# Kernel optimization log

Hardware: AMD Instinct MI355X
Metric: run time of the kernel (lower is better)

Reference implementation:

```python
import jax, jax.numpy as jnp
import numpy as np

B, S, IN, H, OUT, L = 64, 512, 512, 1024, 512, 2


def setup_inputs() -> dict:
    key = jax.random.key(0)
    ks = jax.random.split(key, 12)
    s_in = 1.0 / np.sqrt(IN)
    s_h = 1.0 / np.sqrt(H)
    inp = {
        "x": jax.random.normal(ks[0], (B, S, IN), dtype=jnp.float32),
        "h0": jnp.zeros((B, L, H), dtype=jnp.float32),
        # layer 0: gates stacked [z; r; g] along first axis
        "Wx0": jax.random.uniform(ks[1], (3 * H, IN), minval=-s_in, maxval=s_in),
        "Wh0": jax.random.uniform(ks[2], (3 * H, H), minval=-s_h, maxval=s_h),
        "bh0": jax.random.uniform(ks[3], (3 * H,), minval=-s_h, maxval=s_h),
        # layer 1 (input dim is H)
        "Wx1": jax.random.uniform(ks[4], (3 * H, H), minval=-s_h, maxval=s_h),
        "Wh1": jax.random.uniform(ks[5], (3 * H, H), minval=-s_h, maxval=s_h),
        "bh1": jax.random.uniform(ks[6], (3 * H,), minval=-s_h, maxval=s_h),
        # output projection fc_hy
        "Why": jax.random.uniform(ks[7], (OUT, H), minval=-s_h, maxval=s_h),
        "by": jax.random.uniform(ks[8], (OUT,), minval=-s_h, maxval=s_h),
    }
    return inp


def _gru_layer(x, h_init, Wx, Wh, bh):
    """x: [B,S,D], h_init: [B,H]. Returns (ys [B,S,H], h_final [B,H])."""
    # Batch the input-side projections for all timesteps at once.
    xp = jnp.einsum("bsd,gd->bsg", x, Wx)  # [B,S,3H]
    xz, xr, xg = jnp.split(xp, 3, axis=-1)
    Whz, Whr, Whg = jnp.split(Wh, 3, axis=0)
    bhz, bhr, bhg = jnp.split(bh, 3, axis=0)

    def step(h, xs):
        xz_t, xr_t, xg_t = xs  # each [B,H]
        z = jax.nn.sigmoid(xz_t + h @ Whz.T + bhz)
        r = jax.nn.sigmoid(xr_t + h @ Whr.T + bhr)
        g = jnp.tanh(xg_t + (r * h) @ Whg.T + bhg)
        h_new = z * h + (1.0 - z) * g
        return h_new, h_new

    # time-major scan
    xs = (xz.transpose(1, 0, 2), xr.transpose(1, 0, 2), xg.transpose(1, 0, 2))
    h_final, ys = jax.lax.scan(step, h_init, xs)
    return ys.transpose(1, 0, 2), h_final  # [B,S,H], [B,H]


def reference(x, h0, Wx0, Wh0, bh0, Wx1, Wh1, bh1, Why, by):
    # dropout rate is 0 -> dropout is identity
    y0, hf0 = _gru_layer(x, h0[:, 0, :], Wx0, Wh0, bh0)
    y1, hf1 = _gru_layer(y0, h0[:, 1, :], Wx1, Wh1, bh1)
    layer_output = jnp.einsum("bsh,oh->bso", y1, Why) + by  # [B,S,OUT]
    hidden_state = jnp.stack([hf0, hf1], axis=1)  # [B,L,H]
    return layer_output, jax.lax.stop_gradient(hidden_state)
```

## Files before the change

### kernel.cpp

```cpp
#include <hip/hip_runtime.h>
#include <hip/hip_bf16.h>

#define B_   64
#define S_   512
#define IN_  512
#define H_   1024
#define OUT_ 512
#define H3_  3072
#define TC_  32
#define TCL2 5
#define NCHUNK (S_ / TC_)
#define MC_  (B_ * TC_)
#define NROW (B_ * S_)

#define NBLK 128
#define NTHR 512
#define EXN  32768
#define FPAD 16
#define STAGE_OFF 0
#define HOWN_OFF  32768
#define ZOWN_OFF  36928
#define SMEM_BYTES 41088

typedef float f32x4 __attribute__((ext_vector_type(4)));
typedef short bf16x8 __attribute__((ext_vector_type(8)));
typedef unsigned int u32;
typedef u32 u32x4 __attribute__((ext_vector_type(4)));

struct ChainArgs {
  const float* xp;
  const __hip_bfloat16* Wh;
  float* hf;
  u32* hbuf;
  u32* rhbuf;
  u32* fA;
  u32* fB;
  __hip_bfloat16* y;
  u32 baseA, baseB;
  int t0;
  int layer;
  int active;
  int stagger;
};

__device__ __forceinline__ u32 f2bf_bits(float v) {
  union { __hip_bfloat16 b; unsigned short s; } cv;
  cv.b = __float2bfloat16(v);
  return (u32)cv.s;
}

__device__ __forceinline__ void coh_st(u32* p, u32 v) {
  __hip_atomic_store(p, v, __ATOMIC_RELAXED, __HIP_MEMORY_SCOPE_AGENT);
}
__device__ __forceinline__ u32 coh_ld(const u32* p) {
  return __hip_atomic_load(p, __ATOMIC_RELAXED, __HIP_MEMORY_SCOPE_AGENT);
}

__device__ __forceinline__ void waitflags(const u32* f, int rgbase, u32 target) {
  const u32* my = f + (size_t)(rgbase + (threadIdx.x & 15)) * FPAD;
  int it = 0;
  while (true) {
    u32 v = coh_ld(my);
    if (__all((int)(v >= target))) break;
    if (it < 2) {
      __builtin_amdgcn_s_sleep(2);
    } else {
      __builtin_amdgcn_s_sleep(8);
    }
    ++it;
  }
  __builtin_amdgcn_sched_barrier(0);
}

__device__ __forceinline__ void stage_ex(const u32* __restrict__ src, char* stage, int tid,
                                         int rg) {
  u32x4 v[4];
#pragma unroll
  for (int i = 0; i < 4; ++i) {
    int c4 = tid + i * NTHR;
    int cgp = c4 >> 7;
    int s = c4 & 127;
    const u32* p = src + (((size_t)(cgp * 4 + rg) * 16 + (s >> 3)) * 32 + (s & 7) * 4);
    asm volatile("global_load_dwordx4 %0, %1, off sc0 sc1" : "=v"(v[i]) : "v"(p));
  }
  asm volatile("s_waitcnt vmcnt(0)" ::: "memory");
#pragma unroll
  for (int i = 0; i < 4; ++i) {
    int c4 = tid + i * NTHR;
    int cgp = c4 >> 7;
    int s = c4 & 127;
    int r = s >> 3;
    *(u32x4*)(stage + r * 2048 + ((cgp * 128 + (s & 7) * 16) ^ ((r & 7) << 4))) = v[i];
  }
}

__global__ __launch_bounds__(256) void cast_f32_to_bf16(const float* __restrict__ in,
                                                        __hip_bfloat16* __restrict__ out,
                                                        int n4) {
  int i = blockIdx.x * 256 + threadIdx.x;
  if (i >= n4) return;
  float4 v = ((const float4*)in)[i];
  out[4 * i + 0] = __float2bfloat16(v.x);
  out[4 * i + 1] = __float2bfloat16(v.y);
  out[4 * i + 2] = __float2bfloat16(v.z);
  out[4 * i + 3] = __float2bfloat16(v.w);
}

__global__ __launch_bounds__(256) void gather_cast_x(const float* __restrict__ x,
                                                     __hip_bfloat16* __restrict__ out, int t0) {
  int i = blockIdx.x * 256 + threadIdx.x;
  int e = i * 4;
  int b = e >> 14;
  int rem = e & 16383;
  float4 v = *(const float4*)(x + (size_t)b * (S_ * IN_) + (size_t)t0 * IN_ + rem);
  out[e + 0] = __float2bfloat16(v.x);
  out[e + 1] = __float2bfloat16(v.y);
  out[e + 2] = __float2bfloat16(v.z);
  out[e + 3] = __float2bfloat16(v.w);
}

template <bool REMAP>
__global__ __launch_bounds__(256) void gemm_nt_bias(const __hip_bfloat16* __restrict__ A,
                                                    const __hip_bfloat16* __restrict__ Bm,
                                                    const float* __restrict__ bias,
                                                    float* __restrict__ C, int M, int N, int K,
                                                    int t0) {
  const int lane = threadIdx.x & 63;
  const int w = threadIdx.x >> 6;
  const int wr = w >> 1, wc = w & 1;
  const int row0 = blockIdx.y * 128 + wr * 64;
  const int col0 = blockIdx.x * 128 + wc * 64;
  const int kl = (lane >> 4) * 8;
  const int m16 = lane & 15;
  f32x4 acc[4][4] = {};
  for (int k0 = 0; k0 < K; k0 += 32) {
    bf16x8 a[4], b[4];
#pragma unroll
    for (int i = 0; i < 4; ++i)
      a[i] = *(const bf16x8*)(A + (size_t)(row0 + i * 16 + m16) * K + k0 + kl);
#pragma unroll
    for (int j = 0; j < 4; ++j)
      b[j] = *(const bf16x8*)(Bm + (size_t)(col0 + j * 16 + m16) * K + k0 + kl);
#pragma unroll
    for (int i = 0; i < 4; ++i)
#pragma unroll
      for (int j = 0; j < 4; ++j)
        acc[i][j] = __builtin_amdgcn_mfma_f32_16x16x32_bf16(a[i], b[j], acc[i][j], 0, 0, 0);
  }
  const int rsub = (lane >> 4) * 4;
#pragma unroll
  for (int i = 0; i < 4; ++i) {
    int row = row0 + i * 16 + rsub;
#pragma unroll
    for (int j = 0; j < 4; ++j) {
      int col = col0 + j * 16 + m16;
      float bv = bias[col];
#pragma unroll
      for (int r = 0; r < 4; ++r) {
        int rr = row + r;
        int crow = REMAP ? ((rr >> TCL2) * S_ + t0 + (rr & (TC_ - 1))) : rr;
        C[(size_t)crow * N + col] = acc[i][j][r] + bv;
      }
    }
  }
}

__device__ __forceinline__ void chain_scan(const ChainArgs& ca, const float* __restrict__ h0,
                                           float* __restrict__ hid_out, char* smem, int bx) {
  char* stage = smem + STAGE_OFF;
  float* h_own = (float*)(smem + HOWN_OFF);
  float* z_own = (float*)(smem + ZOWN_OFF);

  const int tid = threadIdx.x;
  const int lane = tid & 63;
  const int w = tid >> 6;
  const int wc = w & 3;
  const int isR = w >> 2;
  const int rg = bx >> 4;
  const int cg = bx & 15;
  const int fid = bx;
  const int rgbase = rg * 16;
  const int m16 = lane & 15;
  const int kl = (lane >> 4) * 8;
  const int rsub = (lane >> 4) * 4;
  const int swzA = (m16 & 7) << 4;
  const int cloc = wc * 16 + m16;

  const float* xp = ca.xp;
  const __hip_bfloat16* Wh = ca.Wh;
  u32* hbuf = ca.hbuf;
  u32* rhbuf = ca.rhbuf;
  u32* flagA = ca.fA;
  u32* flagB = ca.fB;
  const u32 baseA = ca.baseA, baseB = ca.baseB;
  const int t0 = ca.t0, layer = ca.layer;

  for (int i = 0; i < ca.stagger; ++i) __builtin_amdgcn_s_sleep(16);

  {
    int row = tid >> 5, pp = tid & 31;
    int col = cg * 64 + pp * 2;
    int grow = rg * 16 + row;
    float v0, v1;
    if (t0 == 0) {
      v0 = h0[((size_t)grow * 2 + layer) * H_ + col];
      v1 = h0[((size_t)grow * 2 + layer) * H_ + col + 1];
      coh_st(hbuf + EXN + (((size_t)(cg * 4 + rg) * 16 + row) * 32 + pp),
             f2bf_bits(v0) | (f2bf_bits(v1) << 16));
    } else {
      v0 = ca.hf[grow * H_ + col];
      v1 = ca.hf[grow * H_ + col + 1];
    }
    h_own[row * 65 + pp * 2] = v0;
    h_own[row * 65 + pp * 2 + 1] = v1;
  }
  asm volatile("s_waitcnt vmcnt(0)" ::: "memory");
  __syncthreads();
  if (tid == 0) coh_st(flagB + (size_t)fid * FPAD, baseB + 1);

  for (int t = 0; t < TC_; ++t) {
    const int par = t & 1;
    const int colA = cg * 64 + cloc + (isR ? H_ : 0);
    float xpv[4], xpg[4];
#pragma unroll
    for (int j = 0; j < 4; ++j) {
      int grow = rg * 16 + rsub + j;
      xpv[j] = xp[((size_t)(grow * TC_ + t)) * H3_ + colA];
    }
    if (w < 4) {
#pragma unroll
      for (int j = 0; j < 4; ++j) {
        int grow = rg * 16 + rsub + j;
        xpg[j] = xp[((size_t)(grow * TC_ + t)) * H3_ + 2 * H_ + cg * 64 + cloc];
      }
    }

    waitflags(flagB, rgbase, baseB + 1 + t);
    stage_ex(hbuf + (par ^ 1) * EXN, stage, tid, rg);
    __syncthreads();
    {
      f32x4 acc0 = {}, acc1 = {};
      const char* abase = stage + m16 * 2048;
      const __hip_bfloat16* Bb = Wh + (size_t)colA * H_;
#pragma unroll
      for (int k0 = 0; k0 < H_; k0 += 64) {
        bf16x8 a0 = *(const bf16x8*)(abase + (((k0 + kl) * 2) ^ swzA));
        bf16x8 a1 = *(const bf16x8*)(abase + (((k0 + 32 + kl) * 2) ^ swzA));
        bf16x8 b0 = *(const bf16x8*)(Bb + k0 + kl);
        bf16x8 b1 = *(const bf16x8*)(Bb + k0 + 32 + kl);
        acc0 = __builtin_amdgcn_mfma_f32_16x16x32_bf16(a0, b0, acc0, 0, 0, 0);
        acc1 = __builtin_amdgcn_mfma_f32_16x16x32_bf16(a1, b1, acc1, 0, 0, 0);
      }
      if (!isR) {
#pragma unroll
        for (int j = 0; j < 4; ++j) {
          float pre = acc0[j] + acc1[j] + xpv[j];
          z_own[(rsub + j) * 65 + cloc] = 1.f / (1.f + expf(-pre));
        }
      } else {
#pragma unroll
        for (int j = 0; j < 4; ++j) {
          int lr = rsub + j;
          float pre = acc0[j] + acc1[j] + xpv[j];
          float s = 1.f / (1.f + expf(-pre));
          float rh = s * h_own[lr * 65 + cloc];
          u32 bits = f2bf_bits(rh);
          u32 pair = bits | (((u32)__shfl_down((int)bits, 1)) << 16);
          if ((m16 & 1) == 0)
            coh_st(rhbuf + par * EXN + (((size_t)(cg * 4 + rg) * 16 + lr) * 32 + (cloc >> 1)),
                   pair);
        }
        asm volatile("s_waitcnt vmcnt(0)" ::: "memory");
      }
    }
    __syncthreads();
    if (tid == 0) coh_st(flagA + (size_t)fid * FPAD, baseA + t + 1);

    waitflags(flagA, rgbase, baseA + t + 1);
    stage_ex(rhbuf + par * EXN, stage, tid, rg);
    __syncthreads();
    if (w < 4) {
      f32x4 acc0 = {}, acc1 = {};
      const char* abase = stage + m16 * 2048;
      const __hip_bfloat16* Bb = Wh + (size_t)(2 * H_ + cg * 64 + cloc) * H_;
#pragma unroll
      for (int k0 = 0; k0 < H_; k0 += 64) {
        bf16x8 a0 = *(const bf16x8*)(abase + (((k0 + kl) * 2) ^ swzA));
        bf16x8 a1 = *(const bf16x8*)(abase + (((k0 + 32 + kl) * 2) ^ swzA));
        bf16x8 b0 = *(const bf16x8*)(Bb + k0 + kl);
        bf16x8 b1 = *(const bf16x8*)(Bb + k0 + 32 + kl);
        acc0 = __builtin_amdgcn_mfma_f32_16x16x32_bf16(a0, b0, acc0, 0, 0, 0);
        acc1 = __builtin_amdgcn_mfma_f32_16x16x32_bf16(a1, b1, acc1, 0, 0, 0);
      }
#pragma unroll
      for (int j = 0; j < 4; ++j) {
        int lr = rsub + j;
        float pre = acc0[j] + acc1[j] + xpg[j];
        float gg = tanhf(pre);
        float zz = z_own[lr * 65 + cloc];
        float hv = h_own[lr * 65 + cloc];
        float hn = zz * hv + (1.f - zz) * gg;
        h_own[lr * 65 + cloc] = hn;
        u32 bits = f2bf_bits(hn);
        u32 pair = bits | (((u32)__shfl_down((int)bits, 1)) << 16);
        if ((m16 & 1) == 0)
          coh_st(hbuf + par * EXN + (((size_t)(cg * 4 + rg) * 16 + lr) * 32 + (cloc >> 1)), pair);
        ca.y[((size_t)((rg * 16 + lr) * TC_ + t)) * H_ + cg * 64 + cloc] = __float2bfloat16(hn);
      }
      asm volatile("s_waitcnt vmcnt(0)" ::: "memory");
    }
    __syncthreads();
    if (tid == 0) coh_st(flagB + (size_t)fid * FPAD, baseB + t + 2);
  }

  {
    int row = tid >> 5, pp = tid & 31;
    int col = cg * 64 + pp * 2;
    int grow = rg * 16 + row;
    float v0 = h_own[row * 65 + pp * 2];
    float v1 = h_own[row * 65 + pp * 2 + 1];
    ca.hf[grow * H_ + col] = v0;
    ca.hf[grow * H_ + col + 1] = v1;
    if (t0 + TC_ == S_) {
      hid_out[((size_t)grow * 2 + layer) * H_ + col] = v0;
      hid_out[((size_t)grow * 2 + layer) * H_ + col + 1] = v1;
    }
  }
}

__global__ __launch_bounds__(NTHR) void gru_scan_fused(ChainArgs a0, ChainArgs a1,
                                                       const float* __restrict__ h0,
                                                       float* __restrict__ hid_out) {
  extern __shared__ char smem[];
  if (blockIdx.x < 64) {
    if (!a0.active) return;
    chain_scan(a0, h0, hid_out, smem, blockIdx.x);
  } else {
    if (!a1.active) return;
    chain_scan(a1, h0, hid_out, smem, blockIdx.x - 64);
  }
}

extern "C" void kernel_launch(void* const* d_in, const int* in_sizes, int n_in,
                              void* d_out, int out_size, void* d_ws, size_t ws_size,
                              hipStream_t stream) {
  const float* x   = (const float*)d_in[0];
  const float* h0  = (const float*)d_in[1];
  const float* Wx0 = (const float*)d_in[2];
  const float* Wh0 = (const float*)d_in[3];
  const float* bh0 = (const float*)d_in[4];
  const float* Wx1 = (const float*)d_in[5];
  const float* Wh1 = (const float*)d_in[6];
  const float* bh1 = (const float*)d_in[7];
  const float* Why = (const float*)d_in[8];
  const float* by  = (const float*)d_in[9];
  float* out = (float*)d_out;
  float* hid_out = out + (size_t)NROW * OUT_;

  (void)hipFuncSetAttribute((const void*)gru_scan_fused,
                            hipFuncAttributeMaxDynamicSharedMemorySize, SMEM_BYTES);

  char* ws = (char*)d_ws;
  size_t off = 0;
  auto alloc = [&](size_t bytes) {
    char* p = ws + off;
    off += (bytes + 255) & ~(size_t)255;
    return p;
  };
  __hip_bfloat16* wx0b = (__hip_bfloat16*)alloc((size_t)H3_ * IN_ * 2);
  __hip_bfloat16* wh0b = (__hip_bfloat16*)alloc((size_t)H3_ * H_ * 2);
  __hip_bfloat16* wx1b = (__hip_bfloat16*)alloc((size_t)H3_ * H_ * 2);
  __hip_bfloat16* wh1b = (__hip_bfloat16*)alloc((size_t)H3_ * H_ * 2);
  __hip_bfloat16* whyb = (__hip_bfloat16*)alloc((size_t)OUT_ * H_ * 2);
  float* h_f32_0 = (float*)alloc((size_t)B_ * H_ * 4);
  float* h_f32_1 = (float*)alloc((size_t)B_ * H_ * 4);
  u32* hbuf_0  = (u32*)alloc((size_t)2 * EXN * 4);
  u32* hbuf_1  = (u32*)alloc((size_t)2 * EXN * 4);
  u32* rhbuf_0 = (u32*)alloc((size_t)2 * EXN * 4);
  u32* rhbuf_1 = (u32*)alloc((size_t)2 * EXN * 4);
  __hip_bfloat16* x_bfc = (__hip_bfloat16*)alloc((size_t)MC_ * IN_ * 2);
  __hip_bfloat16* y0buf = (__hip_bfloat16*)alloc((size_t)MC_ * H_ * 2);
  __hip_bfloat16* y1buf = (__hip_bfloat16*)alloc((size_t)MC_ * H_ * 2);
  float* xp0buf = (float*)alloc((size_t)MC_ * H3_ * 4);
  float* xp1buf = (float*)alloc((size_t)MC_ * H3_ * 4);
  u32* flags    = (u32*)alloc(4 * 256 * FPAD * 4);
  (void)ws_size;

  (void)hipMemsetAsync(flags, 0, 4 * 256 * FPAD * 4, stream);

  auto cast = [&](const float* in, __hip_bfloat16* o, size_t n) {
    cast_f32_to_bf16<<<dim3((unsigned)((n / 4 + 255) / 256)), dim3(256), 0, stream>>>(in, o,
                                                                                     (int)(n / 4));
  };
  cast(Wx0, wx0b, (size_t)H3_ * IN_);
  cast(Wh0, wh0b, (size_t)H3_ * H_);
  cast(Wx1, wx1b, (size_t)H3_ * H_);
  cast(Wh1, wh1b, (size_t)H3_ * H_);
  cast(Why, whyb, (size_t)OUT_ * H_);

  u32* fA0 = flags;
  u32* fB0 = flags + 256 * FPAD;
  u32* fA1 = flags + 512 * FPAD;
  u32* fB1 = flags + 768 * FPAD;

  auto mkchain = [&](int layer, int chunk, int active) {
    ChainArgs ca;
    int cc = chunk < 0 ? 0 : chunk;
    ca.xp = layer == 0 ? xp0buf : xp1buf;
    ca.Wh = layer == 0 ? wh0b : wh1b;
    ca.hf = layer == 0 ? h_f32_0 : h_f32_1;
    ca.hbuf = layer == 0 ? hbuf_0 : hbuf_1;
    ca.rhbuf = layer == 0 ? rhbuf_0 : rhbuf_1;
    ca.fA = layer == 0 ? fA0 : fA1;
    ca.fB = layer == 0 ? fB0 : fB1;
    ca.y = layer == 0 ? y0buf : y1buf;
    ca.baseA = (u32)cc * TC_;
    ca.baseB = (u32)cc * (TC_ + 1);
    ca.t0 = cc * TC_;
    ca.layer = layer;
    ca.active = active;
    ca.stagger = (layer == 1) ? 14 : 0;
    return ca;
  };

  gather_cast_x<<<dim3(MC_ * IN_ / 4 / 256), dim3(256), 0, stream>>>(x, x_bfc, 0);
  gemm_nt_bias<false><<<dim3(H3_ / 128, MC_ / 128), dim3(256), 0, stream>>>(
      x_bfc, wx0b, bh0, xp0buf, MC_, H3_, IN_, 0);

  for (int c = 0; c <= NCHUNK; ++c) {
    ChainArgs a0 = mkchain(0, c, c < NCHUNK ? 1 : 0);
    ChainArgs a1 = mkchain(1, c - 1, c > 0 ? 1 : 0);
    {
      void* args[] = {(void*)&a0, (void*)&a1, (void*)&h0, (void*)&hid_out};
      hipError_t e = hipLaunchCooperativeKernel((void*)gru_scan_fused, dim3(NBLK), dim3(NTHR),
                                                args, SMEM_BYTES, stream);
      if (e != hipSuccess) {
        (void)hipGetLastError();
        gru_scan_fused<<<dim3(NBLK), dim3(NTHR), SMEM_BYTES, stream>>>(a0, a1, h0, hid_out);
      }
    }
    if (c < NCHUNK) {
      gemm_nt_bias<false><<<dim3(H3_ / 128, MC_ / 128), dim3(256), 0, stream>>>(
          y0buf, wx1b, bh1, xp1buf, MC_, H3_, H_, 0);
    }
    if (c + 1 < NCHUNK) {
      gather_cast_x<<<dim3(MC_ * IN_ / 4 / 256), dim3(256), 0, stream>>>(x, x_bfc, (c + 1) * TC_);
      gemm_nt_bias<false><<<dim3(H3_ / 128, MC_ / 128), dim3(256), 0, stream>>>(
          x_bfc, wx0b, bh0, xp0buf, MC_, H3_, IN_, 0);
    }
    if (c > 0) {
      gemm_nt_bias<true><<<dim3(OUT_ / 128, MC_ / 128), dim3(256), 0, stream>>>(
          y1buf, whyb, by, out, MC_, OUT_, H_, (c - 1) * TC_);
    }
  }
}
```

Baseline: 10.82 ms.

## Stage exchanged hidden slices per producer on flag arrival instead of waiting for all

```diff
diff --git a/kernel.cpp b/kernel.cpp
--- a/kernel.cpp
+++ b/kernel.cpp
@@ -36,6 +36,8 @@
   u32* fA;
   u32* fB;
   __hip_bfloat16* y;
+  const float* h0;
+  float* hid_out;
   u32 baseA, baseB;
   int t0;
   int layer;
@@ -52,46 +54,41 @@
 __device__ __forceinline__ void coh_st(u32* p, u32 v) {
   __hip_atomic_store(p, v, __ATOMIC_RELAXED, __HIP_MEMORY_SCOPE_AGENT);
 }
-__device__ __forceinline__ u32 coh_ld(const u32* p) {
-  return __hip_atomic_load(p, __ATOMIC_RELAXED, __HIP_MEMORY_SCOPE_AGENT);
-}
-
-__device__ __forceinline__ void waitflags(const u32* f, int rgbase, u32 target) {
-  const u32* my = f + (size_t)(rgbase + (threadIdx.x & 15)) * FPAD;
-  int it = 0;
-  while (true) {
-    u32 v = coh_ld(my);
-    if (__all((int)(v >= target))) break;
-    if (it < 2) {
-      __builtin_amdgcn_s_sleep(2);
-    } else {
-      __builtin_amdgcn_s_sleep(8);
-    }
-    ++it;
+
+__device__ __forceinline__ void stage_arrival(const u32* __restrict__ f, int rgbase, u32 target,
+                                              const u32* __restrict__ src, char* stage, int rg) {
+  const int lane = threadIdx.x & 63;
+  const int w = threadIdx.x >> 6;
+#pragma unroll
+  for (int pi = 0; pi < 2; ++pi) {
+    const int p = 2 * w + pi;
+    const u32* fp = f + (size_t)(rgbase + p) * FPAD;
+    int it = 0;
+    while (true) {
+      u32 v;
+      asm volatile("global_load_dword %0, %1, off sc0 sc1\n\ts_waitcnt vmcnt(0)"
+                   : "=v"(v) : "v"(fp) : "memory");
+      if (__all((int)(v >= target))) break;
+      if (it < 4) {
+        __builtin_amdgcn_s_sleep(1);
+      } else {
+        __builtin_amdgcn_s_sleep(4);
+      }
+      ++it;
+    }
+    const u32* sp = src + ((size_t)(p * 4 + rg) * 16) * 32;
+    u32x4 v0, v1;
+    asm volatile("global_load_dwordx4 %0, %1, off sc0 sc1" : "=v"(v0) : "v"(sp + (size_t)lane * 4));
+    asm volatile("global_load_dwordx4 %0, %1, off sc0 sc1"
+                 : "=v"(v1) : "v"(sp + (size_t)(lane + 64) * 4));
+    asm volatile("s_waitcnt vmcnt(0)" ::: "memory");
+    int k = lane, r = k >> 3;
+    *(u32x4*)(stage + r * 2048 + ((p * 128 + (k & 7) * 16) ^ ((r & 7) << 4))) = v0;
+    k = lane + 64;
+    r = k >> 3;
+    *(u32x4*)(stage + r * 2048 + ((p * 128 + (k & 7) * 16) ^ ((r & 7) << 4))) = v1;
   }
   __builtin_amdgcn_sched_barrier(0);
-}
-
-__device__ __forceinline__ void stage_ex(const u32* __restrict__ src, char* stage, int tid,
-                                         int rg) {
-  u32x4 v[4];
-#pragma unroll
-  for (int i = 0; i < 4; ++i) {
-    int c4 = tid + i * NTHR;
-    int cgp = c4 >> 7;
-    int s = c4 & 127;
-    const u32* p = src + (((size_t)(cgp * 4 + rg) * 16 + (s >> 3)) * 32 + (s & 7) * 4);
-    asm volatile("global_load_dwordx4 %0, %1, off sc0 sc1" : "=v"(v[i]) : "v"(p));
-  }
-  asm volatile("s_waitcnt vmcnt(0)" ::: "memory");
-#pragma unroll
-  for (int i = 0; i < 4; ++i) {
-    int c4 = tid + i * NTHR;
-    int cgp = c4 >> 7;
-    int s = c4 & 127;
-    int r = s >> 3;
-    *(u32x4*)(stage + r * 2048 + ((cgp * 128 + (s & 7) * 16) ^ ((r & 7) << 4))) = v[i];
-  }
 }
 
 __global__ __launch_bounds__(256) void cast_f32_to_bf16(const float* __restrict__ in,
@@ -165,8 +162,7 @@
   }
 }
 
-__device__ __forceinline__ void chain_scan(const ChainArgs& ca, const float* __restrict__ h0,
-                                           float* __restrict__ hid_out, char* smem, int bx) {
+__device__ void chain_scan(const ChainArgs& ca, char* smem, int bx) {
   char* stage = smem + STAGE_OFF;
   float* h_own = (float*)(smem + HOWN_OFF);
   float* z_own = (float*)(smem + ZOWN_OFF);
@@ -203,8 +199,8 @@
     int grow = rg * 16 + row;
     float v0, v1;
     if (t0 == 0) {
-      v0 = h0[((size_t)grow * 2 + layer) * H_ + col];
-      v1 = h0[((size_t)grow * 2 + layer) * H_ + col + 1];
+      v0 = ca.h0[((size_t)grow * 2 + layer) * H_ + col];
+      v1 = ca.h0[((size_t)grow * 2 + layer) * H_ + col + 1];
       coh_st(hbuf + EXN + (((size_t)(cg * 4 + rg) * 16 + row) * 32 + pp),
              f2bf_bits(v0) | (f2bf_bits(v1) << 16));
     } else {
@@ -214,9 +210,11 @@
     h_own[row * 65 + pp * 2] = v0;
     h_own[row * 65 + pp * 2 + 1] = v1;
   }
-  asm volatile("s_waitcnt vmcnt(0)" ::: "memory");
-  __syncthreads();
-  if (tid == 0) coh_st(flagB + (size_t)fid * FPAD, baseB + 1);
+  if (t0 == 0) {
+    asm volatile("s_waitcnt vmcnt(0)" ::: "memory");
+    __syncthreads();
+    if (tid == 0) coh_st(flagB + (size_t)fid * FPAD, baseB + 1);
+  }
 
   for (int t = 0; t < TC_; ++t) {
     const int par = t & 1;
@@ -235,8 +233,7 @@
       }
     }
 
-    waitflags(flagB, rgbase, baseB + 1 + t);
-    stage_ex(hbuf + (par ^ 1) * EXN, stage, tid, rg);
+    stage_arrival(flagB, rgbase, baseB + 1 + t, hbuf + (par ^ 1) * EXN, stage, rg);
     __syncthreads();
     {
       f32x4 acc0 = {}, acc1 = {};
@@ -276,8 +273,7 @@
     __syncthreads();
     if (tid == 0) coh_st(flagA + (size_t)fid * FPAD, baseA + t + 1);
 
-    waitflags(flagA, rgbase, baseA + t + 1);
-    stage_ex(rhbuf + par * EXN, stage, tid, rg);
+    stage_arrival(flagA, rgbase, baseA + t + 1, rhbuf + par * EXN, stage, rg);
     __syncthreads();
     if (w < 4) {
       f32x4 acc0 = {}, acc1 = {};
@@ -322,22 +318,20 @@
     ca.hf[grow * H_ + col] = v0;
     ca.hf[grow * H_ + col + 1] = v1;
     if (t0 + TC_ == S_) {
-      hid_out[((size_t)grow * 2 + layer) * H_ + col] = v0;
-      hid_out[((size_t)grow * 2 + layer) * H_ + col + 1] = v1;
-    }
-  }
-}
-
-__global__ __launch_bounds__(NTHR) void gru_scan_fused(ChainArgs a0, ChainArgs a1,
-                                                       const float* __restrict__ h0,
-                                                       float* __restrict__ hid_out) {
+      ca.hid_out[((size_t)grow * 2 + layer) * H_ + col] = v0;
+      ca.hid_out[((size_t)grow * 2 + layer) * H_ + col + 1] = v1;
+    }
+  }
+}
+
+__global__ __launch_bounds__(NTHR) void gru_scan_fused(ChainArgs a0, ChainArgs a1) {
   extern __shared__ char smem[];
   if (blockIdx.x < 64) {
     if (!a0.active) return;
-    chain_scan(a0, h0, hid_out, smem, blockIdx.x);
+    chain_scan(a0, smem, blockIdx.x);
   } else {
     if (!a1.active) return;
-    chain_scan(a1, h0, hid_out, smem, blockIdx.x - 64);
+    chain_scan(a1, smem, blockIdx.x - 64);
   }
 }
 
@@ -414,8 +408,10 @@
     ca.fA = layer == 0 ? fA0 : fA1;
     ca.fB = layer == 0 ? fB0 : fB1;
     ca.y = layer == 0 ? y0buf : y1buf;
+    ca.h0 = h0;
+    ca.hid_out = hid_out;
     ca.baseA = (u32)cc * TC_;
-    ca.baseB = (u32)cc * (TC_ + 1);
+    ca.baseB = (u32)cc * TC_;
     ca.t0 = cc * TC_;
     ca.layer = layer;
     ca.active = active;
@@ -431,12 +427,12 @@
     ChainArgs a0 = mkchain(0, c, c < NCHUNK ? 1 : 0);
     ChainArgs a1 = mkchain(1, c - 1, c > 0 ? 1 : 0);
     {
-      void* args[] = {(void*)&a0, (void*)&a1, (void*)&h0, (void*)&hid_out};
+      void* args[] = {(void*)&a0, (void*)&a1};
       hipError_t e = hipLaunchCooperativeKernel((void*)gru_scan_fused, dim3(NBLK), dim3(NTHR),
                                                 args, SMEM_BYTES, stream);
       if (e != hipSuccess) {
         (void)hipGetLastError();
-        gru_scan_fused<<<dim3(NBLK), dim3(NTHR), SMEM_BYTES, stream>>>(a0, a1, h0, hid_out);
+        gru_scan_fused<<<dim3(NBLK), dim3(NTHR), SMEM_BYTES, stream>>>(a0, a1);
       }
     }
     if (c < NCHUNK) {
```

After: 10.99 ms. No clear change (+1.6%).

## Co-locate both GRU layer chains in one 1024-thread block with soft barriers

Applied to the files above, without the earlier changes.

```diff
diff --git a/kernel.cpp b/kernel.cpp
--- a/kernel.cpp
+++ b/kernel.cpp
@@ -13,14 +13,16 @@
 #define MC_  (B_ * TC_)
 #define NROW (B_ * S_)
 
-#define NBLK 128
-#define NTHR 512
+#define NBLK 64
+#define NTHR 1024
+#define CTHR 512
 #define EXN  32768
 #define FPAD 16
 #define STAGE_OFF 0
 #define HOWN_OFF  32768
 #define ZOWN_OFF  36928
-#define SMEM_BYTES 41088
+#define HALF_     41088
+#define SMEM_BYTES (2 * HALF_)
 
 typedef float f32x4 __attribute__((ext_vector_type(4)));
 typedef short bf16x8 __attribute__((ext_vector_type(8)));
@@ -36,6 +38,8 @@
   u32* fA;
   u32* fB;
   __hip_bfloat16* y;
+  const float* h0;
+  float* hid_out;
   u32 baseA, baseB;
   int t0;
   int layer;
@@ -52,15 +56,24 @@
 __device__ __forceinline__ void coh_st(u32* p, u32 v) {
   __hip_atomic_store(p, v, __ATOMIC_RELAXED, __HIP_MEMORY_SCOPE_AGENT);
 }
-__device__ __forceinline__ u32 coh_ld(const u32* p) {
-  return __hip_atomic_load(p, __ATOMIC_RELAXED, __HIP_MEMORY_SCOPE_AGENT);
-}
-
-__device__ __forceinline__ void waitflags(const u32* f, int rgbase, u32 target) {
-  const u32* my = f + (size_t)(rgbase + (threadIdx.x & 15)) * FPAD;
+
+__device__ __forceinline__ void soft_bar(u32* cnt, u32& bt) {
+  bt += 8;
+  asm volatile("s_waitcnt vmcnt(0) lgkmcnt(0)" ::: "memory");
+  if ((threadIdx.x & 63) == 0) atomicAdd(cnt, 1u);
+  while (__hip_atomic_load(cnt, __ATOMIC_RELAXED, __HIP_MEMORY_SCOPE_WORKGROUP) < bt) {
+    __builtin_amdgcn_s_sleep(1);
+  }
+  __builtin_amdgcn_sched_barrier(0);
+}
+
+__device__ __forceinline__ void waitflags(const u32* f, int rgbase, u32 target, int tl) {
+  const u32* my = f + (size_t)(rgbase + (tl & 15)) * FPAD;
   int it = 0;
   while (true) {
-    u32 v = coh_ld(my);
+    u32 v;
+    asm volatile("global_load_dword %0, %1, off sc0 sc1\n\ts_waitcnt vmcnt(0)"
+                 : "=v"(v) : "v"(my) : "memory");
     if (__all((int)(v >= target))) break;
     if (it < 2) {
       __builtin_amdgcn_s_sleep(2);
@@ -72,12 +85,12 @@
   __builtin_amdgcn_sched_barrier(0);
 }
 
-__device__ __forceinline__ void stage_ex(const u32* __restrict__ src, char* stage, int tid,
+__device__ __forceinline__ void stage_ex(const u32* __restrict__ src, char* stage, int tl,
                                          int rg) {
   u32x4 v[4];
 #pragma unroll
   for (int i = 0; i < 4; ++i) {
-    int c4 = tid + i * NTHR;
+    int c4 = tl + i * CTHR;
     int cgp = c4 >> 7;
     int s = c4 & 127;
     const u32* p = src + (((size_t)(cgp * 4 + rg) * 16 + (s >> 3)) * 32 + (s & 7) * 4);
@@ -86,7 +99,7 @@
   asm volatile("s_waitcnt vmcnt(0)" ::: "memory");
 #pragma unroll
   for (int i = 0; i < 4; ++i) {
-    int c4 = tid + i * NTHR;
+    int c4 = tl + i * CTHR;
     int cgp = c4 >> 7;
     int s = c4 & 127;
     int r = s >> 3;
@@ -165,15 +178,13 @@
   }
 }
 
-__device__ __forceinline__ void chain_scan(const ChainArgs& ca, const float* __restrict__ h0,
-                                           float* __restrict__ hid_out, char* smem, int bx) {
+__device__ void chain_scan(const ChainArgs& ca, char* smem, int bx, int tl, u32* cnt) {
   char* stage = smem + STAGE_OFF;
   float* h_own = (float*)(smem + HOWN_OFF);
   float* z_own = (float*)(smem + ZOWN_OFF);
 
-  const int tid = threadIdx.x;
-  const int lane = tid & 63;
-  const int w = tid >> 6;
+  const int lane = tl & 63;
+  const int w = tl >> 6;
   const int wc = w & 3;
   const int isR = w >> 2;
   const int rg = bx >> 4;
@@ -194,17 +205,18 @@
   u32* flagB = ca.fB;
   const u32 baseA = ca.baseA, baseB = ca.baseB;
   const int t0 = ca.t0, layer = ca.layer;
+  u32 bt = 0;
 
   for (int i = 0; i < ca.stagger; ++i) __builtin_amdgcn_s_sleep(16);
 
   {
-    int row = tid >> 5, pp = tid & 31;
+    int row = tl >> 5, pp = tl & 31;
     int col = cg * 64 + pp * 2;
     int grow = rg * 16 + row;
     float v0, v1;
     if (t0 == 0) {
-      v0 = h0[((size_t)grow * 2 + layer) * H_ + col];
-      v1 = h0[((size_t)grow * 2 + layer) * H_ + col + 1];
+      v0 = ca.h0[((size_t)grow * 2 + layer) * H_ + col];
+      v1 = ca.h0[((size_t)grow * 2 + layer) * H_ + col + 1];
       coh_st(hbuf + EXN + (((size_t)(cg * 4 + rg) * 16 + row) * 32 + pp),
              f2bf_bits(v0) | (f2bf_bits(v1) << 16));
     } else {
@@ -214,9 +226,8 @@
     h_own[row * 65 + pp * 2] = v0;
     h_own[row * 65 + pp * 2 + 1] = v1;
   }
-  asm volatile("s_waitcnt vmcnt(0)" ::: "memory");
-  __syncthreads();
-  if (tid == 0) coh_st(flagB + (size_t)fid * FPAD, baseB + 1);
+  soft_bar(cnt, bt);
+  if (tl == 0) coh_st(flagB + (size_t)fid * FPAD, baseB + 1);
 
   for (int t = 0; t < TC_; ++t) {
     const int par = t & 1;
@@ -235,9 +246,9 @@
       }
     }
 
-    waitflags(flagB, rgbase, baseB + 1 + t);
-    stage_ex(hbuf + (par ^ 1) * EXN, stage, tid, rg);
-    __syncthreads();
+    waitflags(flagB, rgbase, baseB + 1 + t, tl);
+    stage_ex(hbuf + (par ^ 1) * EXN, stage, tl, rg);
+    soft_bar(cnt, bt);
     {
       f32x4 acc0 = {}, acc1 = {};
       const char* abase = stage + m16 * 2048;
@@ -270,15 +281,14 @@
             coh_st(rhbuf + par * EXN + (((size_t)(cg * 4 + rg) * 16 + lr) * 32 + (cloc >> 1)),
                    pair);
         }
-        asm volatile("s_waitcnt vmcnt(0)" ::: "memory");
-      }
-    }
-    __syncthreads();
-    if (tid == 0) coh_st(flagA + (size_t)fid * FPAD, baseA + t + 1);
-
-    waitflags(flagA, rgbase, baseA + t + 1);
-    stage_ex(rhbuf + par * EXN, stage, tid, rg);
-    __syncthreads();
+      }
+    }
+    soft_bar(cnt, bt);
+    if (tl == 0) coh_st(flagA + (size_t)fid * FPAD, baseA + t + 1);
+
+    waitflags(flagA, rgbase, baseA + t + 1, tl);
+    stage_ex(rhbuf + par * EXN, stage, tl, rg);
+    soft_bar(cnt, bt);
     if (w < 4) {
       f32x4 acc0 = {}, acc1 = {};
       const char* abase = stage + m16 * 2048;
@@ -307,14 +317,13 @@
           coh_st(hbuf + par * EXN + (((size_t)(cg * 4 + rg) * 16 + lr) * 32 + (cloc >> 1)), pair);
         ca.y[((size_t)((rg * 16 + lr) * TC_ + t)) * H_ + cg * 64 + cloc] = __float2bfloat16(hn);
       }
-      asm volatile("s_waitcnt vmcnt(0)" ::: "memory");
-    }
-    __syncthreads();
-    if (tid == 0) coh_st(flagB + (size_t)fid * FPAD, baseB + t + 2);
+    }
+    soft_bar(cnt, bt);
+    if (tl == 0) coh_st(flagB + (size_t)fid * FPAD, baseB + t + 2);
   }
 
   {
-    int row = tid >> 5, pp = tid & 31;
+    int row = tl >> 5, pp = tl & 31;
     int col = cg * 64 + pp * 2;
     int grow = rg * 16 + row;
     float v0 = h_own[row * 65 + pp * 2];
@@ -322,22 +331,26 @@
     ca.hf[grow * H_ + col] = v0;
     ca.hf[grow * H_ + col + 1] = v1;
     if (t0 + TC_ == S_) {
-      hid_out[((size_t)grow * 2 + layer) * H_ + col] = v0;
-      hid_out[((size_t)grow * 2 + layer) * H_ + col + 1] = v1;
-    }
-  }
-}
-
-__global__ __launch_bounds__(NTHR) void gru_scan_fused(ChainArgs a0, ChainArgs a1,
-                                                       const float* __restrict__ h0,
-                                                       float* __restrict__ hid_out) {
+      ca.hid_out[((size_t)grow * 2 + layer) * H_ + col] = v0;
+      ca.hid_out[((size_t)grow * 2 + layer) * H_ + col + 1] = v1;
+    }
+  }
+}
+
+__global__ __launch_bounds__(NTHR) void gru_scan_fused(ChainArgs a0, ChainArgs a1) {
   extern __shared__ char smem[];
-  if (blockIdx.x < 64) {
+  __shared__ u32 bar_cnt[2];
+  const int tid = threadIdx.x;
+  if (tid < 2) bar_cnt[tid] = 0;
+  __syncthreads();
+  const int chain = tid >> 9;
+  const int tl = tid & 511;
+  if (chain == 0) {
     if (!a0.active) return;
-    chain_scan(a0, h0, hid_out, smem, blockIdx.x);
+    chain_scan(a0, smem, blockIdx.x, tl, &bar_cnt[0]);
   } else {
     if (!a1.active) return;
-    chain_scan(a1, h0, hid_out, smem, blockIdx.x - 64);
+    chain_scan(a1, smem + HALF_, blockIdx.x, tl, &bar_cnt[1]);
   }
 }
 
@@ -414,6 +427,8 @@
     ca.fA = layer == 0 ? fA0 : fA1;
     ca.fB = layer == 0 ? fB0 : fB1;
     ca.y = layer == 0 ? y0buf : y1buf;
+    ca.h0 = h0;
+    ca.hid_out = hid_out;
     ca.baseA = (u32)cc * TC_;
     ca.baseB = (u32)cc * (TC_ + 1);
     ca.t0 = cc * TC_;
@@ -431,12 +446,12 @@
     ChainArgs a0 = mkchain(0, c, c < NCHUNK ? 1 : 0);
     ChainArgs a1 = mkchain(1, c - 1, c > 0 ? 1 : 0);
     {
-      void* args[] = {(void*)&a0, (void*)&a1, (void*)&h0, (void*)&hid_out};
+      void* args[] = {(void*)&a0, (void*)&a1};
       hipError_t e = hipLaunchCooperativeKernel((void*)gru_scan_fused, dim3(NBLK), dim3(NTHR),
                                                 args, SMEM_BYTES, stream);
       if (e != hipSuccess) {
         (void)hipGetLastError();
-        gru_scan_fused<<<dim3(NBLK), dim3(NTHR), SMEM_BYTES, stream>>>(a0, a1, h0, hid_out);
+        gru_scan_fused<<<dim3(NBLK), dim3(NTHR), SMEM_BYTES, stream>>>(a0, a1);
       }
     }
     if (c < NCHUNK) {
```

Result: slower. 19.39 ms (+79.2%).

## Halve scan blocks so each block interleaves two row groups

Applied to the files above, without the earlier changes.

```diff
diff --git a/kernel.cpp b/kernel.cpp
--- a/kernel.cpp
+++ b/kernel.cpp
@@ -13,14 +13,16 @@
 #define MC_  (B_ * TC_)
 #define NROW (B_ * S_)
 
-#define NBLK 128
+#define NBLK 64
 #define NTHR 512
 #define EXN  32768
 #define FPAD 16
 #define STAGE_OFF 0
-#define HOWN_OFF  32768
-#define ZOWN_OFF  36928
-#define SMEM_BYTES 41088
+#define HOWN0_OFF 32768
+#define ZOWN0_OFF 36928
+#define HOWN1_OFF 41088
+#define ZOWN1_OFF 45248
+#define SMEM_BYTES 49408
 
 typedef float f32x4 __attribute__((ext_vector_type(4)));
 typedef short bf16x8 __attribute__((ext_vector_type(8)));
@@ -36,11 +38,12 @@
   u32* fA;
   u32* fB;
   __hip_bfloat16* y;
+  const float* h0;
+  float* hid_out;
   u32 baseA, baseB;
   int t0;
   int layer;
   int active;
-  int stagger;
 };
 
 __device__ __forceinline__ u32 f2bf_bits(float v) {
@@ -52,15 +55,14 @@
 __device__ __forceinline__ void coh_st(u32* p, u32 v) {
   __hip_atomic_store(p, v, __ATOMIC_RELAXED, __HIP_MEMORY_SCOPE_AGENT);
 }
-__device__ __forceinline__ u32 coh_ld(const u32* p) {
-  return __hip_atomic_load(p, __ATOMIC_RELAXED, __HIP_MEMORY_SCOPE_AGENT);
-}
 
 __device__ __forceinline__ void waitflags(const u32* f, int rgbase, u32 target) {
   const u32* my = f + (size_t)(rgbase + (threadIdx.x & 15)) * FPAD;
   int it = 0;
   while (true) {
-    u32 v = coh_ld(my);
+    u32 v;
+    asm volatile("global_load_dword %0, %1, off sc0 sc1\n\ts_waitcnt vmcnt(0)"
+                 : "=v"(v) : "v"(my) : "memory");
     if (__all((int)(v >= target))) break;
     if (it < 2) {
       __builtin_amdgcn_s_sleep(2);
@@ -165,21 +167,17 @@
   }
 }
 
-__device__ __forceinline__ void chain_scan(const ChainArgs& ca, const float* __restrict__ h0,
-                                           float* __restrict__ hid_out, char* smem, int bx) {
+__device__ void chain_scan(const ChainArgs& ca, char* smem, int p, int cg) {
   char* stage = smem + STAGE_OFF;
-  float* h_own = (float*)(smem + HOWN_OFF);
-  float* z_own = (float*)(smem + ZOWN_OFF);
+  float* h_own[2] = {(float*)(smem + HOWN0_OFF), (float*)(smem + HOWN1_OFF)};
+  float* z_own[2] = {(float*)(smem + ZOWN0_OFF), (float*)(smem + ZOWN1_OFF)};
+  const int rgs[2] = {p, p + 2};
 
   const int tid = threadIdx.x;
   const int lane = tid & 63;
   const int w = tid >> 6;
   const int wc = w & 3;
   const int isR = w >> 2;
-  const int rg = bx >> 4;
-  const int cg = bx & 15;
-  const int fid = bx;
-  const int rgbase = rg * 16;
   const int m16 = lane & 15;
   const int kl = (lane >> 4) * 8;
   const int rsub = (lane >> 4) * 4;
@@ -195,149 +193,167 @@
   const u32 baseA = ca.baseA, baseB = ca.baseB;
   const int t0 = ca.t0, layer = ca.layer;
 
-  for (int i = 0; i < ca.stagger; ++i) __builtin_amdgcn_s_sleep(16);
-
-  {
+#pragma unroll
+  for (int s = 0; s < 2; ++s) {
+    int rg = rgs[s];
     int row = tid >> 5, pp = tid & 31;
     int col = cg * 64 + pp * 2;
     int grow = rg * 16 + row;
     float v0, v1;
     if (t0 == 0) {
-      v0 = h0[((size_t)grow * 2 + layer) * H_ + col];
-      v1 = h0[((size_t)grow * 2 + layer) * H_ + col + 1];
+      v0 = ca.h0[((size_t)grow * 2 + layer) * H_ + col];
+      v1 = ca.h0[((size_t)grow * 2 + layer) * H_ + col + 1];
       coh_st(hbuf + EXN + (((size_t)(cg * 4 + rg) * 16 + row) * 32 + pp),
              f2bf_bits(v0) | (f2bf_bits(v1) << 16));
     } else {
       v0 = ca.hf[grow * H_ + col];
       v1 = ca.hf[grow * H_ + col + 1];
     }
-    h_own[row * 65 + pp * 2] = v0;
-    h_own[row * 65 + pp * 2 + 1] = v1;
+    h_own[s][row * 65 + pp * 2] = v0;
+    h_own[s][row * 65 + pp * 2 + 1] = v1;
   }
   asm volatile("s_waitcnt vmcnt(0)" ::: "memory");
   __syncthreads();
-  if (tid == 0) coh_st(flagB + (size_t)fid * FPAD, baseB + 1);
+  if (tid == 0) {
+    coh_st(flagB + (size_t)(rgs[0] * 16 + cg) * FPAD, baseB + 1);
+    coh_st(flagB + (size_t)(rgs[1] * 16 + cg) * FPAD, baseB + 1);
+  }
 
   for (int t = 0; t < TC_; ++t) {
     const int par = t & 1;
-    const int colA = cg * 64 + cloc + (isR ? H_ : 0);
-    float xpv[4], xpg[4];
-#pragma unroll
-    for (int j = 0; j < 4; ++j) {
-      int grow = rg * 16 + rsub + j;
-      xpv[j] = xp[((size_t)(grow * TC_ + t)) * H3_ + colA];
-    }
-    if (w < 4) {
+
+#pragma unroll
+    for (int s = 0; s < 2; ++s) {
+      const int rg = rgs[s];
+      const int colA = cg * 64 + cloc + (isR ? H_ : 0);
+      float xpv[4];
 #pragma unroll
       for (int j = 0; j < 4; ++j) {
         int grow = rg * 16 + rsub + j;
-        xpg[j] = xp[((size_t)(grow * TC_ + t)) * H3_ + 2 * H_ + cg * 64 + cloc];
-      }
-    }
-
-    waitflags(flagB, rgbase, baseB + 1 + t);
-    stage_ex(hbuf + (par ^ 1) * EXN, stage, tid, rg);
-    __syncthreads();
-    {
-      f32x4 acc0 = {}, acc1 = {};
-      const char* abase = stage + m16 * 2048;
-      const __hip_bfloat16* Bb = Wh + (size_t)colA * H_;
-#pragma unroll
-      for (int k0 = 0; k0 < H_; k0 += 64) {
-        bf16x8 a0 = *(const bf16x8*)(abase + (((k0 + kl) * 2) ^ swzA));
-        bf16x8 a1 = *(const bf16x8*)(abase + (((k0 + 32 + kl) * 2) ^ swzA));
-        bf16x8 b0 = *(const bf16x8*)(Bb + k0 + kl);
-        bf16x8 b1 = *(const bf16x8*)(Bb + k0 + 32 + kl);
-        acc0 = __builtin_amdgcn_mfma_f32_16x16x32_bf16(a0, b0, acc0, 0, 0, 0);
-        acc1 = __builtin_amdgcn_mfma_f32_16x16x32_bf16(a1, b1, acc1, 0, 0, 0);
-      }
-      if (!isR) {
+        xpv[j] = xp[((size_t)(grow * TC_ + t)) * H3_ + colA];
+      }
+      waitflags(flagB, rg * 16, baseB + 1 + t);
+      stage_ex(hbuf + (par ^ 1) * EXN, stage, tid, rg);
+      __syncthreads();
+      {
+        f32x4 acc0 = {}, acc1 = {};
+        const char* abase = stage + m16 * 2048;
+        const __hip_bfloat16* Bb = Wh + (size_t)colA * H_;
+#pragma unroll
+        for (int k0 = 0; k0 < H_; k0 += 64) {
+          bf16x8 a0 = *(const bf16x8*)(abase + (((k0 + kl) * 2) ^ swzA));
+          bf16x8 a1 = *(const bf16x8*)(abase + (((k0 + 32 + kl) * 2) ^ swzA));
+          bf16x8 b0 = *(const bf16x8*)(Bb + k0 + kl);
+          bf16x8 b1 = *(const bf16x8*)(Bb + k0 + 32 + kl);
+          acc0 = __builtin_amdgcn_mfma_f32_16x16x32_bf16(a0, b0, acc0, 0, 0, 0);
+          acc1 = __builtin_amdgcn_mfma_f32_16x16x32_bf16(a1, b1, acc1, 0, 0, 0);
+        }
+        if (!isR) {
+#pragma unroll
+          for (int j = 0; j < 4; ++j) {
+            float pre = acc0[j] + acc1[j] + xpv[j];
+            z_own[s][(rsub + j) * 65 + cloc] = 1.f / (1.f + expf(-pre));
+          }
+        } else {
+#pragma unroll
+          for (int j = 0; j < 4; ++j) {
+            int lr = rsub + j;
+            float pre = acc0[j] + acc1[j] + xpv[j];
+            float sg = 1.f / (1.f + expf(-pre));
+            float rh = sg * h_own[s][lr * 65 + cloc];
+            u32 bits = f2bf_bits(rh);
+            u32 pair = bits | (((u32)__shfl_down((int)bits, 1)) << 16);
+            if ((m16 & 1) == 0)
+              coh_st(rhbuf + par * EXN + (((size_t)(cg * 4 + rg) * 16 + lr) * 32 + (cloc >> 1)),
+                     pair);
+          }
+          asm volatile("s_waitcnt vmcnt(0)" ::: "memory");
+        }
+      }
+      __syncthreads();
+      if (tid == 0) coh_st(flagA + (size_t)(rg * 16 + cg) * FPAD, baseA + t + 1);
+    }
+
+#pragma unroll
+    for (int s = 0; s < 2; ++s) {
+      const int rg = rgs[s];
+      float xpg[4];
+      if (w < 4) {
 #pragma unroll
         for (int j = 0; j < 4; ++j) {
-          float pre = acc0[j] + acc1[j] + xpv[j];
-          z_own[(rsub + j) * 65 + cloc] = 1.f / (1.f + expf(-pre));
+          int grow = rg * 16 + rsub + j;
+          xpg[j] = xp[((size_t)(grow * TC_ + t)) * H3_ + 2 * H_ + cg * 64 + cloc];
         }
-      } else {
+      }
+      waitflags(flagA, rg * 16, baseA + t + 1);
+      stage_ex(rhbuf + par * EXN, stage, tid, rg);
+      __syncthreads();
+      if (w < 4) {
+        f32x4 acc0 = {}, acc1 = {};
+        const char* abase = stage + m16 * 2048;
+        const __hip_bfloat16* Bb = Wh + (size_t)(2 * H_ + cg * 64 + cloc) * H_;
+#pragma unroll
+        for (int k0 = 0; k0 < H_; k0 += 64) {
+          bf16x8 a0 = *(const bf16x8*)(abase + (((k0 + kl) * 2) ^ swzA));
+          bf16x8 a1 = *(const bf16x8*)(abase + (((k0 + 32 + kl) * 2) ^ swzA));
+          bf16x8 b0 = *(const bf16x8*)(Bb + k0 + kl);
+          bf16x8 b1 = *(const bf16x8*)(Bb + k0 + 32 + kl);
+          acc0 = __builtin_amdgcn_mfma_f32_16x16x32_bf16(a0, b0, acc0, 0, 0, 0);
+          acc1 = __builtin_amdgcn_mfma_f32_16x16x32_bf16(a1, b1, acc1, 0, 0, 0);
+        }
 #pragma unroll
         for (int j = 0; j < 4; ++j) {
           int lr = rsub + j;
-          float pre = acc0[j] + acc1[j] + xpv[j];
-          float s = 1.f / (1.f + expf(-pre));
-          float rh = s * h_own[lr * 65 + cloc];
-          u32 bits = f2bf_bits(rh);
+          float pre = acc0[j] + acc1[j] + xpg[j];
+          float gg = tanhf(pre);
+          float zz = z_own[s][lr * 65 + cloc];
+          float hv = h_own[s][lr * 65 + cloc];
+          float hn = zz * hv + (1.f - zz) * gg;
+          h_own[s][lr * 65 + cloc] = hn;
+          u32 bits = f2bf_bits(hn);
           u32 pair = bits | (((u32)__shfl_down((int)bits, 1)) << 16);
           if ((m16 & 1) == 0)
-            coh_st(rhbuf + par * EXN + (((size_t)(cg * 4 + rg) * 16 + lr) * 32 + (cloc >> 1)),
+            coh_st(hbuf + par * EXN + (((size_t)(cg * 4 + rg) * 16 + lr) * 32 + (cloc >> 1)),
                    pair);
+          ca.y[((size_t)((rg * 16 + lr) * TC_ + t)) * H_ + cg * 64 + cloc] = __float2bfloat16(hn);
         }
         asm volatile("s_waitcnt vmcnt(0)" ::: "memory");
       }
-    }
-    __syncthreads();
-    if (tid == 0) coh_st(flagA + (size_t)fid * FPAD, baseA + t + 1);
-
-    waitflags(flagA, rgbase, baseA + t + 1);
-    stage_ex(rhbuf + par * EXN, stage, tid, rg);
-    __syncthreads();
-    if (w < 4) {
-      f32x4 acc0 = {}, acc1 = {};
-      const char* abase = stage + m16 * 2048;
-      const __hip_bfloat16* Bb = Wh + (size_t)(2 * H_ + cg * 64 + cloc) * H_;
-#pragma unroll
-      for (int k0 = 0; k0 < H_; k0 += 64) {
-        bf16x8 a0 = *(const bf16x8*)(abase + (((k0 + kl) * 2) ^ swzA));
-        bf16x8 a1 = *(const bf16x8*)(abase + (((k0 + 32 + kl) * 2) ^ swzA));
-        bf16x8 b0 = *(const bf16x8*)(Bb + k0 + kl);
-        bf16x8 b1 = *(const bf16x8*)(Bb + k0 + 32 + kl);
-        acc0 = __builtin_amdgcn_mfma_f32_16x16x32_bf16(a0, b0, acc0, 0, 0, 0);
-        acc1 = __builtin_amdgcn_mfma_f32_16x16x32_bf16(a1, b1, acc1, 0, 0, 0);
-      }
-#pragma unroll
-      for (int j = 0; j < 4; ++j) {
-        int lr = rsub + j;
-        float pre = acc0[j] + acc1[j] + xpg[j];
-        float gg = tanhf(pre);
-        float zz = z_own[lr * 65 + cloc];
-        float hv = h_own[lr * 65 + cloc];
-        float hn = zz * hv + (1.f - zz) * gg;
-        h_own[lr * 65 + cloc] = hn;
-        u32 bits = f2bf_bits(hn);
-        u32 pair = bits | (((u32)__shfl_down((int)bits, 1)) << 16);
-        if ((m16 & 1) == 0)
-          coh_st(hbuf + par * EXN + (((size_t)(cg * 4 + rg) * 16 + lr) * 32 + (cloc >> 1)), pair);
-        ca.y[((size_t)((rg * 16 + lr) * TC_ + t)) * H_ + cg * 64 + cloc] = __float2bfloat16(hn);
-      }
-      asm volatile("s_waitcnt vmcnt(0)" ::: "memory");
-    }
-    __syncthreads();
-    if (tid == 0) coh_st(flagB + (size_t)fid * FPAD, baseB + t + 2);
-  }
-
-  {
+      __syncthreads();
+      if (tid == 0) coh_st(flagB + (size_t)(rg * 16 + cg) * FPAD, baseB + t + 2);
+    }
+  }
+
+#pragma unroll
+  for (int s = 0; s < 2; ++s) {
+    int rg = rgs[s];
     int row = tid >> 5, pp = tid & 31;
     int col = cg * 64 + pp * 2;
     int grow = rg * 16 + row;
-    float v0 = h_own[row * 65 + pp * 2];
-    float v1 = h_own[row * 65 + pp * 2 + 1];
+    float v0 = h_own[s][row * 65 + pp * 2];
+    float v1 = h_own[s][row * 65 + pp * 2 + 1];
     ca.hf[grow * H_ + col] = v0;
     ca.hf[grow * H_ + col + 1] = v1;
     if (t0 + TC_ == S_) {
-      hid_out[((size_t)grow * 2 + layer) * H_ + col] = v0;
-      hid_out[((size_t)grow * 2 + layer) * H_ + col + 1] = v1;
-    }
-  }
-}
-
-__global__ __launch_bounds__(NTHR) void gru_scan_fused(ChainArgs a0, ChainArgs a1,
-                                                       const float* __restrict__ h0,
-                                                       float* __restrict__ hid_out) {
+      ca.hid_out[((size_t)grow * 2 + layer) * H_ + col] = v0;
+      ca.hid_out[((size_t)grow * 2 + layer) * H_ + col + 1] = v1;
+    }
+  }
+}
+
+__global__ __launch_bounds__(NTHR) void gru_scan_fused(ChainArgs a0, ChainArgs a1) {
   extern __shared__ char smem[];
-  if (blockIdx.x < 64) {
+  const int bx = blockIdx.x;
+  const int chain = bx >> 5;
+  const int b5 = bx & 31;
+  const int p = b5 >> 4;
+  const int cg = b5 & 15;
+  if (chain == 0) {
     if (!a0.active) return;
-    chain_scan(a0, h0, hid_out, smem, blockIdx.x);
+    chain_scan(a0, smem, p, cg);
   } else {
     if (!a1.active) return;
-    chain_scan(a1, h0, hid_out, smem, blockIdx.x - 64);
+    chain_scan(a1, smem, p, cg);
   }
 }
 
@@ -414,12 +430,13 @@
     ca.fA = layer == 0 ? fA0 : fA1;
     ca.fB = layer == 0 ? fB0 : fB1;
     ca.y = layer == 0 ? y0buf : y1buf;
+    ca.h0 = h0;
+    ca.hid_out = hid_out;
     ca.baseA = (u32)cc * TC_;
     ca.baseB = (u32)cc * (TC_ + 1);
     ca.t0 = cc * TC_;
     ca.layer = layer;
     ca.active = active;
-    ca.stagger = (layer == 1) ? 14 : 0;
     return ca;
   };
 
@@ -431,12 +448,12 @@
     ChainArgs a0 = mkchain(0, c, c < NCHUNK ? 1 : 0);
     ChainArgs a1 = mkchain(1, c - 1, c > 0 ? 1 : 0);
     {
-      void* args[] = {(void*)&a0, (void*)&a1, (void*)&h0, (void*)&hid_out};
+      void* args[] = {(void*)&a0, (void*)&a1};
       hipError_t e = hipLaunchCooperativeKernel((void*)gru_scan_fused, dim3(NBLK), dim3(NTHR),
                                                 args, SMEM_BYTES, stream);
       if (e != hipSuccess) {
         (void)hipGetLastError();
-        gru_scan_fused<<<dim3(NBLK), dim3(NTHR), SMEM_BYTES, stream>>>(a0, a1, h0, hid_out);
+        gru_scan_fused<<<dim3(NBLK), dim3(NTHR), SMEM_BYTES, stream>>>(a0, a1);
       }
     }
     if (c < NCHUNK) {
```

Measured after the change: 18.24 ms. +68.6%, slower.
